# Performance work log

Measured on AMD Instinct MI355X. Metric: run time of the kernel, lower is better.

## Reference

```python
import jax, jax.numpy as jnp
import numpy as np

B, S, N, D, M = 4, 4096, 16, 64, 4  # batch, seq, heads, head_dim, num_scales

def setup_inputs() -> dict:
    key = jax.random.key(0)
    ks = jax.random.split(key, 6)
    return {
        "q": jax.random.normal(ks[0], (B, S, N, D), dtype=jnp.float32),
        "k": jax.random.normal(ks[1], (B, S, N, D), dtype=jnp.float32),
        "v": jax.random.normal(ks[2], (B, S, N, D), dtype=jnp.float32),
        "memory": jax.random.normal(ks[3], (B, M, N, D, D), dtype=jnp.float32),
        "decay_factors": jax.random.uniform(ks[4], (M,), dtype=jnp.float32) + 0.5,
        "gate_weights": jax.random.uniform(ks[5], (M,), dtype=jnp.float32),
    }

def reference(q, k, v, memory, decay_factors, gate_weights):
    # --- update_memory: decayed outer-product accumulation ---
    # new_info[b,n,k,v] = sum_s k[b,s,n,k] * v[b,s,n,v]  (fused; never build [b,s,n,k,v])
    new_info = jnp.einsum('bsnk,bsnv->bnkv', k, v)
    sig = jax.nn.sigmoid(decay_factors)            # [M]
    sig5 = sig[None, :, None, None, None]          # [1,M,1,1,1]
    mem_new = memory * sig5 + (1.0 - sig5) * new_info[:, None]  # [B,M,N,D,D]
    # --- forward read: q @ memory per scale, softmax-gated scale mixing ---
    gates = jax.nn.softmax(gate_weights)           # [M]
    # fuse gate mixing into the contraction; never build [b,m,s,n,v]
    out = jnp.einsum('bsnk,bmnkv,m->bsnv', q, mem_new, gates)
    return out
```

## Files before the change

kernel.cpp:

```cpp
#include <hip/hip_runtime.h>
#include <hip/hip_bf16.h>
#include <math.h>

constexpr int B = 4, S = 4096, N = 16, D = 64, M = 4;
constexpr int SND = S * N * D;
constexpr int ND  = N * D;
constexpr int DD  = D * D;
constexpr int NCH = 32;
constexpr int SPB = S / NCH;

typedef __attribute__((ext_vector_type(8))) short bf16x8;
typedef __attribute__((ext_vector_type(4))) float f32x4;
typedef unsigned short u16;
typedef unsigned int u32;

__device__ inline u16 f2bf(float x) {
  __hip_bfloat16 h = __float2bfloat16(x);
  return __builtin_bit_cast(u16, h);
}

__global__ __launch_bounds__(256) void k1_partials(const float* __restrict__ kg,
                                                   const float* __restrict__ vg,
                                                   u16* __restrict__ part) {
  __shared__ u16 kT[64][128];
  __shared__ u16 vT[64][128];

  const int t = threadIdx.x, w = t >> 6, l = t & 63;
  const int lr = l & 15, lg = l >> 4;
  const int rp = t >> 4;
  const int c  = t & 15;
  const int bn = blockIdx.x, ch = blockIdx.y;
  const int b = bn >> 4, n = bn & 15;

  const size_t base = (size_t)b * SND + (size_t)n * D + (size_t)ch * SPB * ND;

  float4 kr[8], vr[8];
#pragma unroll
  for (int st = 0; st < 4; ++st) {
    const float* kp = kg + base + (size_t)(st * 32 + 2 * rp) * ND + 4 * c;
    const float* vp = vg + base + (size_t)(st * 32 + 2 * rp) * ND + 4 * c;
    kr[2 * st]     = *(const float4*)kp;
    kr[2 * st + 1] = *(const float4*)(kp + ND);
    vr[2 * st]     = *(const float4*)vp;
    vr[2 * st + 1] = *(const float4*)(vp + ND);
  }

  __builtin_amdgcn_sched_barrier(0);

#pragma unroll
  for (int st = 0; st < 4; ++st) {
    const int s  = st * 32 + 2 * rp;
    const int so = s >> 3, sl = s & 7;
    const float* k0 = (const float*)&kr[2 * st];
    const float* k1 = (const float*)&kr[2 * st + 1];
    const float* v0 = (const float*)&vr[2 * st];
    const float* v1 = (const float*)&vr[2 * st + 1];
#pragma unroll
    for (int o = 0; o < 4; ++o) {
      const int d = 4 * c + o;
      const int slot = ((so ^ (d & 15)) << 3) + sl;
      *(u32*)&kT[d][slot] = (u32)f2bf(k0[o]) | ((u32)f2bf(k1[o]) << 16);
      *(u32*)&vT[d][slot] = (u32)f2bf(v0[o]) | ((u32)f2bf(v1[o]) << 16);
    }
  }

  __syncthreads();

  f32x4 acc[4];
#pragma unroll
  for (int i = 0; i < 4; ++i) acc[i] = (f32x4)0.f;

#pragma unroll
  for (int kk = 0; kk < 4; ++kk) {
    const int so = 4 * kk + lg;
    const int da = 16 * w + lr;
    bf16x8 af = *(const bf16x8*)&kT[da][(so ^ (da & 15)) << 3];
    bf16x8 bq[4];
#pragma unroll
    for (int ni = 0; ni < 4; ++ni) {
      const int db = 16 * ni + lr;
      bq[ni] = *(const bf16x8*)&vT[db][(so ^ (db & 15)) << 3];
    }
#pragma unroll
    for (int ni = 0; ni < 4; ++ni)
      acc[ni] = __builtin_amdgcn_mfma_f32_16x16x32_bf16(af, bq[ni],
                                                        acc[ni], 0, 0, 0);
  }

  u16* p = part + ((size_t)bn * NCH + ch) * DD;
#pragma unroll
  for (int ni = 0; ni < 4; ++ni)
#pragma unroll
    for (int ri = 0; ri < 4; ++ri)
      p[(16 * w + 4 * lg + ri) * 64 + 16 * ni + lr] = f2bf(acc[ni][ri]);
}

__global__ __launch_bounds__(256) void k2_combine(const u16* __restrict__ part,
                                                  const float* __restrict__ memg,
                                                  const float* __restrict__ decay,
                                                  const float* __restrict__ gatew,
                                                  u16* __restrict__ meffT) {
  const int t = threadIdx.x;
  const int bn = blockIdx.x;
  const int b = bn >> 4, n = bn & 15;
  const int kv = blockIdx.y * 256 + t;
  const int k = kv >> 6, v = kv & 63;

  float gw[M], df[M];
#pragma unroll
  for (int m = 0; m < M; ++m) { gw[m] = gatew[m]; df[m] = decay[m]; }
  const float mx = fmaxf(fmaxf(gw[0], gw[1]), fmaxf(gw[2], gw[3]));
  float e[M], esum = 0.f;
#pragma unroll
  for (int m = 0; m < M; ++m) { e[m] = expf(gw[m] - mx); esum += e[m]; }
  float wgt[M], cc = 0.f;
#pragma unroll
  for (int m = 0; m < M; ++m) {
    const float g = e[m] / esum;
    const float sg = 1.f / (1.f + expf(-df[m]));
    wgt[m] = g * sg;
    cc += g * (1.f - sg);
  }

  const u16* pb = part + (size_t)bn * NCH * DD + kv;
  float ni = 0.f;
#pragma unroll 8
  for (int ch = 0; ch < NCH; ++ch) {
    __hip_bfloat16 h = __builtin_bit_cast(__hip_bfloat16, pb[(size_t)ch * DD]);
    ni += __bfloat162float(h);
  }
  float a = cc * ni;
#pragma unroll
  for (int m = 0; m < M; ++m)
    a += wgt[m] * memg[(((size_t)b * M + m) * N + n) * DD + kv];

  meffT[(size_t)bn * DD + v * 64 + k] = f2bf(a);
}

__global__ __launch_bounds__(256, 4) void k3_out(const float* __restrict__ qg,
                                                 const u16* __restrict__ meffT,
                                                 float* __restrict__ outg) {
  const int t = threadIdx.x, w = t >> 6, l = t & 63;
  const int lr = l & 15, lg = l >> 4;
  const int bn = blockIdx.x;
  const int b = bn >> 4, n = bn & 15;
  const int s0 = blockIdx.y * 256 + w * 64;

  const u16* mb = meffT + (size_t)bn * DD;
  bf16x8 bfr[4][2];
#pragma unroll
  for (int ni = 0; ni < 4; ++ni)
#pragma unroll
    for (int ks = 0; ks < 2; ++ks)
      bfr[ni][ks] = *(const bf16x8*)(mb + (16 * ni + lr) * 64 + 32 * ks + 8 * lg);

  f32x4 acc[4][4];
#pragma unroll
  for (int i = 0; i < 4; ++i)
#pragma unroll
    for (int j = 0; j < 4; ++j) acc[i][j] = (f32x4)0.f;

  const size_t qbase = (size_t)b * SND + (size_t)n * D;

#pragma unroll
  for (int mi = 0; mi < 4; ++mi) {
    const float* qr = qg + qbase + (size_t)(s0 + 16 * mi + lr) * ND + 8 * lg;
#pragma unroll
    for (int ks = 0; ks < 2; ++ks) {
      float qa[8];
      *(float4*)&qa[0] = *(const float4*)(qr + 32 * ks);
      *(float4*)&qa[4] = *(const float4*)(qr + 32 * ks + 4);
      bf16x8 a;
#pragma unroll
      for (int j = 0; j < 8; ++j) a[j] = (short)f2bf(qa[j]);
#pragma unroll
      for (int ni = 0; ni < 4; ++ni)
        acc[mi][ni] = __builtin_amdgcn_mfma_f32_16x16x32_bf16(a, bfr[ni][ks],
                                                              acc[mi][ni], 0, 0, 0);
    }
  }

#pragma unroll
  for (int mi = 0; mi < 4; ++mi)
#pragma unroll
    for (int ni = 0; ni < 4; ++ni)
#pragma unroll
      for (int ri = 0; ri < 4; ++ri)
        outg[qbase + (size_t)(s0 + 16 * mi + 4 * lg + ri) * ND + 16 * ni + lr] =
            acc[mi][ni][ri];
}

extern "C" void kernel_launch(void* const* d_in, const int* in_sizes, int n_in,
                              void* d_out, int out_size, void* d_ws, size_t ws_size,
                              hipStream_t stream) {
  const float* q     = (const float*)d_in[0];
  const float* k     = (const float*)d_in[1];
  const float* v     = (const float*)d_in[2];
  const float* memg  = (const float*)d_in[3];
  const float* decay = (const float*)d_in[4];
  const float* gatew = (const float*)d_in[5];
  float* out = (float*)d_out;

  u16* meffT = (u16*)d_ws;
  const size_t meffT_bytes = (size_t)64 * DD * sizeof(u16);
  u16* part = (u16*)((char*)d_ws + meffT_bytes);

  hipLaunchKernelGGL(k1_partials, dim3(64, NCH), dim3(256), 0, stream,
                     k, v, part);
  hipLaunchKernelGGL(k2_combine, dim3(64, 16), dim3(256), 0, stream,
                     part, memg, decay, gatew, meffT);
  hipLaunchKernelGGL(k3_out, dim3(64, 16), dim3(256), 0, stream,
                     q, meffT, out);
}
```

Baseline: 67.38 us.

## Pipeline k1 with async global-to-LDS triple buffering over fewer chunks

```diff
diff --git a/kernel.cpp b/kernel.cpp
--- a/kernel.cpp
+++ b/kernel.cpp
@@ -6,8 +6,9 @@
 constexpr int SND = S * N * D;
 constexpr int ND  = N * D;
 constexpr int DD  = D * D;
-constexpr int NCH = 32;
+constexpr int NCH = 8;
 constexpr int SPB = S / NCH;
+constexpr int NST = 16;
 
 typedef __attribute__((ext_vector_type(8))) short bf16x8;
 typedef __attribute__((ext_vector_type(4))) float f32x4;
@@ -19,73 +20,82 @@
   return __builtin_bit_cast(u16, h);
 }
 
+__device__ inline void gload16(const float* g, float* l) {
+  __builtin_amdgcn_global_load_lds(
+      (const __attribute__((address_space(1))) void*)g,
+      (__attribute__((address_space(3))) void*)l, 16, 0, 0);
+}
+
 __global__ __launch_bounds__(256) void k1_partials(const float* __restrict__ kg,
                                                    const float* __restrict__ vg,
                                                    u16* __restrict__ part) {
-  __shared__ u16 kT[64][128];
-  __shared__ u16 vT[64][128];
+  __shared__ float kbuf[3][32][64];
+  __shared__ float vbuf[3][32][64];
 
   const int t = threadIdx.x, w = t >> 6, l = t & 63;
   const int lr = l & 15, lg = l >> 4;
-  const int rp = t >> 4;
-  const int c  = t & 15;
   const int bn = blockIdx.x, ch = blockIdx.y;
   const int b = bn >> 4, n = bn & 15;
-
-  const size_t base = (size_t)b * SND + (size_t)n * D + (size_t)ch * SPB * ND;
-
-  float4 kr[8], vr[8];
-#pragma unroll
-  for (int st = 0; st < 4; ++st) {
-    const float* kp = kg + base + (size_t)(st * 32 + 2 * rp) * ND + 4 * c;
-    const float* vp = vg + base + (size_t)(st * 32 + 2 * rp) * ND + 4 * c;
-    kr[2 * st]     = *(const float4*)kp;
-    kr[2 * st + 1] = *(const float4*)(kp + ND);
-    vr[2 * st]     = *(const float4*)vp;
-    vr[2 * st + 1] = *(const float4*)(vp + ND);
-  }
-
+  const size_t base = (size_t)b * SND + (size_t)n * D;
+  const int s0 = ch * SPB;
+
+  f32x4 acc[4];
+#pragma unroll
+  for (int i = 0; i < 4; ++i) acc[i] = (f32x4)0.f;
+
+#define STAGE(st, bi)                                                        \
+  {                                                                          \
+    _Pragma("unroll") for (int i = 0; i < 2; ++i) {                          \
+      const int gid = (w * 2 + i) * 64 + l;              \
+      const int sl = gid >> 4, df = (gid & 15) * 4;                          \
+      const float* gk = kg + base + (size_t)(s0 + (st) * 32 + sl) * ND + df; \
+      const float* gv = vg + base + (size_t)(s0 + (st) * 32 + sl) * ND + df; \
+      gload16(gk, &kbuf[bi][0][0] + (w * 2 + i) * 256);                      \
+      gload16(gv, &vbuf[bi][0][0] + (w * 2 + i) * 256);                      \
+    }                                                                        \
+  }
+
+#define COMPUTE(bi)                                                          \
+  {                                                                          \
+    bf16x8 af, bq[4];                                                        \
+    _Pragma("unroll") for (int j = 0; j < 8; ++j)                            \
+      af[j] = (short)f2bf(kbuf[bi][8 * lg + j][16 * w + lr]);                \
+    _Pragma("unroll") for (int ni = 0; ni < 4; ++ni)                         \
+    _Pragma("unroll") for (int j = 0; j < 8; ++j)                            \
+      bq[ni][j] = (short)f2bf(vbuf[bi][8 * lg + j][16 * ni + lr]);           \
+    _Pragma("unroll") for (int ni = 0; ni < 4; ++ni)                         \
+      acc[ni] = __builtin_amdgcn_mfma_f32_16x16x32_bf16(af, bq[ni],          \
+                                                        acc[ni], 0, 0, 0);   \
+  }
+
+#define WAIT4                                                                \
+  asm volatile("s_waitcnt vmcnt(4) lgkmcnt(0)" ::: "memory");                \
+  __builtin_amdgcn_sched_barrier(0);                                         \
+  __builtin_amdgcn_s_barrier();                                              \
   __builtin_amdgcn_sched_barrier(0);
 
-#pragma unroll
-  for (int st = 0; st < 4; ++st) {
-    const int s  = st * 32 + 2 * rp;
-    const int so = s >> 3, sl = s & 7;
-    const float* k0 = (const float*)&kr[2 * st];
-    const float* k1 = (const float*)&kr[2 * st + 1];
-    const float* v0 = (const float*)&vr[2 * st];
-    const float* v1 = (const float*)&vr[2 * st + 1];
-#pragma unroll
-    for (int o = 0; o < 4; ++o) {
-      const int d = 4 * c + o;
-      const int slot = ((so ^ (d & 15)) << 3) + sl;
-      *(u32*)&kT[d][slot] = (u32)f2bf(k0[o]) | ((u32)f2bf(k1[o]) << 16);
-      *(u32*)&vT[d][slot] = (u32)f2bf(v0[o]) | ((u32)f2bf(v1[o]) << 16);
-    }
-  }
-
-  __syncthreads();
-
-  f32x4 acc[4];
-#pragma unroll
-  for (int i = 0; i < 4; ++i) acc[i] = (f32x4)0.f;
-
-#pragma unroll
-  for (int kk = 0; kk < 4; ++kk) {
-    const int so = 4 * kk + lg;
-    const int da = 16 * w + lr;
-    bf16x8 af = *(const bf16x8*)&kT[da][(so ^ (da & 15)) << 3];
-    bf16x8 bq[4];
-#pragma unroll
-    for (int ni = 0; ni < 4; ++ni) {
-      const int db = 16 * ni + lr;
-      bq[ni] = *(const bf16x8*)&vT[db][(so ^ (db & 15)) << 3];
-    }
-#pragma unroll
-    for (int ni = 0; ni < 4; ++ni)
-      acc[ni] = __builtin_amdgcn_mfma_f32_16x16x32_bf16(af, bq[ni],
-                                                        acc[ni], 0, 0, 0);
-  }
+#define WAIT0                                                                \
+  asm volatile("s_waitcnt vmcnt(0) lgkmcnt(0)" ::: "memory");                \
+  __builtin_amdgcn_sched_barrier(0);                                         \
+  __builtin_amdgcn_s_barrier();                                              \
+  __builtin_amdgcn_sched_barrier(0);
+
+  STAGE(0, 0);
+  STAGE(1, 1);
+  WAIT4;
+
+#pragma unroll
+  for (int st = 0; st < NST; ++st) {
+    if (st + 2 < NST) STAGE(st + 2, (st + 2) % 3);
+    COMPUTE(st % 3);
+    if (st < NST - 2) { WAIT4; }
+    else if (st == NST - 2) { WAIT0; }
+  }
+
+#undef STAGE
+#undef COMPUTE
+#undef WAIT4
+#undef WAIT0
 
   u16* p = part + ((size_t)bn * NCH + ch) * DD;
 #pragma unroll
@@ -124,7 +134,7 @@
 
   const u16* pb = part + (size_t)bn * NCH * DD + kv;
   float ni = 0.f;
-#pragma unroll 8
+#pragma unroll
   for (int ch = 0; ch < NCH; ++ch) {
     __hip_bfloat16 h = __builtin_bit_cast(__hip_bfloat16, pb[(size_t)ch * DD]);
     ni += __bfloat162float(h);
```

New measurement: 60.03 us. 1.12x faster.
